# Performance work log

Hardware: AMD Instinct MI355X
Metric: run time of the kernel (lower is better)

The kernel has to match this reference:

```python
import jax, jax.numpy as jnp
import numpy as np

S, D = 4096, 64
DROPOUT_P = 0.1


def setup_inputs() -> dict:
    key = jax.random.key(0)
    k1, k2, k3, k4, k5, k6 = jax.random.split(key, 6)
    return {
        "query": jax.random.normal(k1, (S, D), dtype=jnp.float32),
        "key": jax.random.normal(k2, (S, D), dtype=jnp.float32),
        "value": jax.random.normal(k3, (S, D), dtype=jnp.float32),
        "u_drop": jax.random.uniform(k4, (S, S), dtype=jnp.float32),
        "row_rand": jax.random.uniform(k5, (S, 1), dtype=jnp.float32),
        "x": jax.random.normal(k6, (1,), dtype=jnp.float32),
    }


def reference(query, key, value, u_drop, row_rand, x):
    d = query.shape[-1]
    # torch code divides by scale_factor = d**-0.5, i.e. multiplies by sqrt(d)
    qk = jnp.matmul(query, key.T) * jnp.asarray(d, query.dtype) ** 0.5  # [S,S]
    # dropout with keep prob (1-p), inverted scaling (matches F.dropout)
    keep = (u_drop >= DROPOUT_P).astype(qk.dtype) / (1.0 - DROPOUT_P)
    t = qk * keep  # [S,S]
    # drop_rows_or_cols: random floor mask normalized by its global sum
    r = jnp.floor(t * row_rand)          # [S,S] (row_rand broadcasts over cols)
    t = t * (r / jnp.sum(r))             # [S,S]
    return jnp.matmul(t, value)          # [S,D]
```

## Files before the change

### kernel.cpp

```cpp
#include <hip/hip_runtime.h>
#include <stdint.h>


#define S 4096
#define D 64
#define NCHUNK 8
#define JCHUNK (S / NCHUNK)
#define JT 128
#define NTILES (JCHUNK / JT)
#define LDP 132
#define KSCALE (8.0f / 0.9f)

typedef float f32x4 __attribute__((ext_vector_type(4)));
typedef short s16x8 __attribute__((ext_vector_type(8)));
typedef unsigned short u16x4 __attribute__((ext_vector_type(4)));
typedef const __attribute__((address_space(1))) unsigned g_u32;
typedef __attribute__((address_space(3))) unsigned lds_u32;

__device__ inline unsigned short f2bf(float f) {
    union { float f; unsigned u; } v; v.f = f;
    unsigned r = v.u + 0x7fffu + ((v.u >> 16) & 1u);
    return (unsigned short)(r >> 16);
}

__global__ void prep_all(const float* __restrict__ Q,
                         const float* __restrict__ Kf,
                         const float* __restrict__ V,
                         short* __restrict__ Qbf, short* __restrict__ Kbf,
                         short* __restrict__ VTbf, int* __restrict__ sumr) {
    __shared__ short tile[64 * 68];
    const int b   = blockIdx.x;
    const int tid = threadIdx.x;
    if (b == 0 && tid == 0) *sumr = 0;

    if (b < 512) {
        const int idx = b * 256 + tid;
        if (idx < 65536) {
            float4 v = ((const float4*)Q)[idx];
            u16x4 o; o[0] = f2bf(v.x); o[1] = f2bf(v.y); o[2] = f2bf(v.z); o[3] = f2bf(v.w);
            ((u16x4*)Qbf)[idx] = o;
        } else {
            const int k = idx - 65536;
            float4 v = ((const float4*)Kf)[k];
            u16x4 o; o[0] = f2bf(v.x * KSCALE); o[1] = f2bf(v.y * KSCALE);
                     o[2] = f2bf(v.z * KSCALE); o[3] = f2bf(v.w * KSCALE);
            ((u16x4*)Kbf)[k] = o;
        }
    } else {
        const int j0 = (b - 512) * 64;
#pragma unroll
        for (int it = 0; it < 4; ++it) {
            const int f4 = tid + it * 256;
            const int row = f4 >> 4, c4 = (f4 & 15) * 4;
            float4 v = *(const float4*)&V[(size_t)(j0 + row) * D + c4];
            tile[(c4 + 0) * 68 + row] = (short)f2bf(v.x);
            tile[(c4 + 1) * 68 + row] = (short)f2bf(v.y);
            tile[(c4 + 2) * 68 + row] = (short)f2bf(v.z);
            tile[(c4 + 3) * 68 + row] = (short)f2bf(v.w);
        }
        __syncthreads();
#pragma unroll
        for (int it = 0; it < 4; ++it) {
            const int f4 = tid + it * 256;
            const int d = f4 >> 4, o4 = (f4 & 15) * 4;
            u16x4 w = *(const u16x4*)&tile[d * 68 + o4];
            *(u16x4*)&VTbf[(size_t)d * S + j0 + o4] = w;
        }
    }
}

__launch_bounds__(256, 2)
__global__ void fused_main(const short* __restrict__ Qbf,
                           const short* __restrict__ Kbf,
                           const short* __restrict__ VTbf,
                           const float* __restrict__ Ud,
                           const float* __restrict__ RR,
                           float* __restrict__ Opart,
                           int* __restrict__ sumr)
{
    __shared__ short kb[2][16 * 512];
    __shared__ short vb[16 * 512];
    __shared__ short pb[4 * 16 * LDP];
    __shared__ int red[4];

    const int tid  = threadIdx.x;
    const int w    = tid >> 6;
    const int lane = tid & 63;
    const int quad = lane >> 4;
    const int n16  = lane & 15;

    const int ib  = blockIdx.x & 63;
    const int ic  = blockIdx.x >> 6;
    const int i0w = ib * 64 + w * 16;
    const int jbase = ic * JCHUNK;

    const float* uwb = Ud + (size_t)i0w * S;

    s16x8 aQ[2];
#pragma unroll
    for (int ks = 0; ks < 2; ++ks)
        aQ[ks] = *(const s16x8*)&Qbf[(size_t)(i0w + n16) * D + ks * 32 + quad * 8];

    float rr[4];
#pragma unroll
    for (int rg = 0; rg < 4; ++rg) rr[rg] = RR[i0w + quad * 4 + rg];

    f32x4 accO[4];
#pragma unroll
    for (int ds = 0; ds < 4; ++ds) accO[ds] = (f32x4){0.f, 0.f, 0.f, 0.f};

    float lsum = 0.f;
    short* pw = pb + w * 16 * LDP;

    unsigned um[2];
    const int bsel  = quad * 4 + (n16 & 3);
    const int bidx0 = (n16 >> 2) * 4;

    float4 un[8];
    {
        const int j0 = jbase;
#pragma unroll
        for (int h = 0; h < 2; ++h)
#pragma unroll
            for (int q = 0; q < 4; ++q)
                un[h * 4 + q] = *(const float4*)&uwb[(size_t)(q * 4 + quad) * S + j0 + h * 64 + n16 * 4];
#pragma unroll
        for (int p = 0; p < 4; ++p) {
            const int e = w * 4 + p;
            __builtin_amdgcn_global_load_lds(
                (g_u32*)&Kbf[(size_t)(j0 + (e >> 1) * 16 + n16) * D + (e & 1) * 32 + quad * 8],
                (lds_u32*)&kb[0][e * 512], 16, 0, 0);
        }
#pragma unroll
        for (int p = 0; p < 4; ++p) {
            const int e = w * 4 + p;
            __builtin_amdgcn_global_load_lds(
                (g_u32*)&VTbf[(size_t)((e & 3) * 16 + n16) * S + j0 + (e >> 2) * 32 + quad * 8],
                (lds_u32*)&vb[e * 512], 16, 0, 0);
        }
        unsigned m = 0;
#pragma unroll
        for (int e = 0; e < 8; ++e) {
            m |= (un[e].x >= 0.1f ? 1u : 0u) << (e * 4 + 0);
            m |= (un[e].y >= 0.1f ? 1u : 0u) << (e * 4 + 1);
            m |= (un[e].z >= 0.1f ? 1u : 0u) << (e * 4 + 2);
            m |= (un[e].w >= 0.1f ? 1u : 0u) << (e * 4 + 3);
        }
        um[0] = m;
    }

#pragma unroll
    for (int jt = 0; jt < NTILES; ++jt) {
        const int bu = jt & 1;
        const int nb = bu ^ 1;
        const int j0 = jbase + jt * JT;
        const bool last = (jt + 1 == NTILES);

        if (!last) {
            const int j1 = j0 + JT;
#pragma unroll
            for (int h = 0; h < 2; ++h)
#pragma unroll
                for (int q = 0; q < 4; ++q)
                    un[h * 4 + q] = *(const float4*)&uwb[(size_t)(q * 4 + quad) * S + j1 + h * 64 + n16 * 4];
#pragma unroll
            for (int p = 0; p < 4; ++p) {
                const int e = w * 4 + p;
                __builtin_amdgcn_global_load_lds(
                    (g_u32*)&Kbf[(size_t)(j1 + (e >> 1) * 16 + n16) * D + (e & 1) * 32 + quad * 8],
                    (lds_u32*)&kb[nb][e * 512], 16, 0, 0);
            }
        }

        if (!last) { __asm__ volatile("s_waitcnt vmcnt(12)" ::: "memory"); }
        else       { __asm__ volatile("s_waitcnt vmcnt(0)"  ::: "memory"); }
        __builtin_amdgcn_s_barrier();
        __asm__ volatile("" ::: "memory");

#pragma unroll
        for (int cs = 0; cs < 8; ++cs) {
            f32x4 acc = (f32x4){0.f, 0.f, 0.f, 0.f};
#pragma unroll
            for (int ks = 0; ks < 2; ++ks) {
                s16x8 bK = *(const s16x8*)&kb[bu][(cs * 2 + ks) * 512 + lane * 8];
                acc = __builtin_amdgcn_mfma_f32_16x16x32_bf16(aQ[ks], bK, acc, 0, 0, 0);
            }
            const int h = cs >> 2, c4 = cs & 3;
#pragma unroll
            for (int rg = 0; rg < 4; ++rg) {
                const int mv = __builtin_amdgcn_ds_bpermute(
                    (rg * 16 + c4 * 4) * 4 + bidx0, (int)um[bu]);
                const float t = ((((unsigned)mv) >> (h * 16 + bsel)) & 1u) ? acc[rg] : 0.0f;
                const float r = floorf(t * rr[rg]);
                lsum += r;
                pw[(quad * 4 + rg) * LDP + cs * 16 + n16] = (short)f2bf(t * r);
            }
        }

        __builtin_amdgcn_wave_barrier();
        __asm__ volatile("s_waitcnt lgkmcnt(0)" ::: "memory");
        __builtin_amdgcn_wave_barrier();

#pragma unroll
        for (int ksj = 0; ksj < 4; ++ksj) {
            s16x8 aP = *(const s16x8*)&pw[n16 * LDP + ksj * 32 + quad * 8];
#pragma unroll
            for (int ds = 0; ds < 4; ++ds) {
                s16x8 bV = *(const s16x8*)&vb[(ksj * 4 + ds) * 512 + lane * 8];
                accO[ds] = __builtin_amdgcn_mfma_f32_16x16x32_bf16(aP, bV, accO[ds], 0, 0, 0);
            }
        }

        __asm__ volatile("" ::: "memory");
        __builtin_amdgcn_s_barrier();
        __asm__ volatile("" ::: "memory");

        if (!last) {
            unsigned m = 0;
#pragma unroll
            for (int e = 0; e < 8; ++e) {
                m |= (un[e].x >= 0.1f ? 1u : 0u) << (e * 4 + 0);
                m |= (un[e].y >= 0.1f ? 1u : 0u) << (e * 4 + 1);
                m |= (un[e].z >= 0.1f ? 1u : 0u) << (e * 4 + 2);
                m |= (un[e].w >= 0.1f ? 1u : 0u) << (e * 4 + 3);
            }
            um[nb] = m;
            const int j1 = j0 + JT;
#pragma unroll
            for (int p = 0; p < 4; ++p) {
                const int e = w * 4 + p;
                __builtin_amdgcn_global_load_lds(
                    (g_u32*)&VTbf[(size_t)((e & 3) * 16 + n16) * S + j1 + (e >> 2) * 32 + quad * 8],
                    (lds_u32*)&vb[e * 512], 16, 0, 0);
            }
        }
    }

    float* op = Opart + (size_t)ic * S * D;
#pragma unroll
    for (int ds = 0; ds < 4; ++ds) {
        const int d = ds * 16 + n16;
#pragma unroll
        for (int rg = 0; rg < 4; ++rg) {
            const int i = i0w + quad * 4 + rg;
            op[(size_t)i * D + d] = accO[ds][rg];
        }
    }

    for (int off = 32; off; off >>= 1) lsum += __shfl_down(lsum, off);
    if (lane == 0) red[w] = (int)lsum;
    __syncthreads();
    if (tid == 0) atomicAdd(sumr, red[0] + red[1] + red[2] + red[3]);
}

__global__ void reduce_out(const float* __restrict__ Opart,
                           const int* __restrict__ sumr,
                           float* __restrict__ out) {
    const int idx = blockIdx.x * 256 + threadIdx.x;
    const float invR = 1.0f / (float)(*sumr);
    float sx = 0.f, sy = 0.f, sz = 0.f, sw = 0.f;
#pragma unroll
    for (int c = 0; c < NCHUNK; ++c) {
        const float4 v = ((const float4*)(Opart + (size_t)c * S * D))[idx];
        sx += v.x; sy += v.y; sz += v.z; sw += v.w;
    }
    float4 o; o.x = sx * invR; o.y = sy * invR; o.z = sz * invR; o.w = sw * invR;
    ((float4*)out)[idx] = o;
}

extern "C" void kernel_launch(void* const* d_in, const int* in_sizes, int n_in,
                              void* d_out, int out_size, void* d_ws, size_t ws_size,
                              hipStream_t stream) {
    (void)in_sizes; (void)n_in; (void)out_size; (void)ws_size;
    const float* Q  = (const float*)d_in[0];
    const float* Kf = (const float*)d_in[1];
    const float* V  = (const float*)d_in[2];
    const float* Ud = (const float*)d_in[3];
    const float* RR = (const float*)d_in[4];
    float* out = (float*)d_out;

    char* ws = (char*)d_ws;
    float* Opart = (float*)ws;
    short* Qbf  = (short*)(ws + (8u << 20));
    short* Kbf  = (short*)(ws + (8u << 20) + (512u << 10));
    short* VTbf = (short*)(ws + (8u << 20) + (1024u << 10));
    int*   sumr = (int*)  (ws + (8u << 20) + (1536u << 10));

    prep_all<<<dim3(576), dim3(256), 0, stream>>>(Q, Kf, V, Qbf, Kbf, VTbf, sumr);
    fused_main<<<dim3(64 * NCHUNK), dim3(256), 0, stream>>>(
        Qbf, Kbf, VTbf, Ud, RR, Opart, sumr);
    reduce_out<<<dim3(256), dim3(256), 0, stream>>>(Opart, sumr, out);
}
```

Before: 121.2 us.

## Pre-pack dropout mask into bitmask in prep kernel, read bits in main kernel

```diff
diff --git a/kernel.cpp b/kernel.cpp
--- a/kernel.cpp
+++ b/kernel.cpp
@@ -10,10 +10,12 @@
 #define NTILES (JCHUNK / JT)
 #define LDP 132
 #define KSCALE (8.0f / 0.9f)
+#define MASKB 2048
 
 typedef float f32x4 __attribute__((ext_vector_type(4)));
 typedef short s16x8 __attribute__((ext_vector_type(8)));
 typedef unsigned short u16x4 __attribute__((ext_vector_type(4)));
+typedef int i32x4 __attribute__((ext_vector_type(4)));
 typedef const __attribute__((address_space(1))) unsigned g_u32;
 typedef __attribute__((address_space(3))) unsigned lds_u32;
 
@@ -26,15 +28,30 @@
 __global__ void prep_all(const float* __restrict__ Q,
                          const float* __restrict__ Kf,
                          const float* __restrict__ V,
+                         const float* __restrict__ Ud,
                          short* __restrict__ Qbf, short* __restrict__ Kbf,
-                         short* __restrict__ VTbf, int* __restrict__ sumr) {
+                         short* __restrict__ VTbf,
+                         unsigned* __restrict__ PM, int* __restrict__ sumr) {
     __shared__ short tile[64 * 68];
     const int b   = blockIdx.x;
     const int tid = threadIdx.x;
     if (b == 0 && tid == 0) *sumr = 0;
 
-    if (b < 512) {
-        const int idx = b * 256 + tid;
+    if (b < MASKB) {
+        const int wi = b * 256 + tid;
+        const float4* src = (const float4*)Ud + (size_t)wi * 8;
+        unsigned m = 0;
+#pragma unroll
+        for (int q = 0; q < 8; ++q) {
+            const float4 v = src[q];
+            m |= (v.x >= 0.1f ? 1u : 0u) << (q * 4 + 0);
+            m |= (v.y >= 0.1f ? 1u : 0u) << (q * 4 + 1);
+            m |= (v.z >= 0.1f ? 1u : 0u) << (q * 4 + 2);
+            m |= (v.w >= 0.1f ? 1u : 0u) << (q * 4 + 3);
+        }
+        PM[wi] = m;
+    } else if (b < MASKB + 512) {
+        const int idx = (b - MASKB) * 256 + tid;
         if (idx < 65536) {
             float4 v = ((const float4*)Q)[idx];
             u16x4 o; o[0] = f2bf(v.x); o[1] = f2bf(v.y); o[2] = f2bf(v.z); o[3] = f2bf(v.w);
@@ -47,7 +64,7 @@
             ((u16x4*)Kbf)[k] = o;
         }
     } else {
-        const int j0 = (b - 512) * 64;
+        const int j0 = (b - MASKB - 512) * 64;
 #pragma unroll
         for (int it = 0; it < 4; ++it) {
             const int f4 = tid + it * 256;
@@ -73,7 +90,7 @@
 __global__ void fused_main(const short* __restrict__ Qbf,
                            const short* __restrict__ Kbf,
                            const short* __restrict__ VTbf,
-                           const float* __restrict__ Ud,
+                           const unsigned* __restrict__ PM,
                            const float* __restrict__ RR,
                            float* __restrict__ Opart,
                            int* __restrict__ sumr)
@@ -94,8 +111,6 @@
     const int i0w = ib * 64 + w * 16;
     const int jbase = ic * JCHUNK;
 
-    const float* uwb = Ud + (size_t)i0w * S;
-
     s16x8 aQ[2];
 #pragma unroll
     for (int ks = 0; ks < 2; ++ks)
@@ -112,41 +127,31 @@
     float lsum = 0.f;
     short* pw = pb + w * 16 * LDP;
 
-    unsigned um[2];
-    const int bsel  = quad * 4 + (n16 & 3);
-    const int bidx0 = (n16 >> 2) * 4;
-
-    float4 un[8];
+    const unsigned* pmr[4];
+#pragma unroll
+    for (int rg = 0; rg < 4; ++rg)
+        pmr[rg] = PM + (size_t)(i0w + quad * 4 + rg) * (S / 32) + (jbase >> 5);
+
+    i32x4 mk[2][4];
+
     {
-        const int j0 = jbase;
-#pragma unroll
-        for (int h = 0; h < 2; ++h)
-#pragma unroll
-            for (int q = 0; q < 4; ++q)
-                un[h * 4 + q] = *(const float4*)&uwb[(size_t)(q * 4 + quad) * S + j0 + h * 64 + n16 * 4];
+#pragma unroll
+        for (int rg = 0; rg < 4; ++rg)
+            mk[0][rg] = *(const i32x4*)pmr[rg];
 #pragma unroll
         for (int p = 0; p < 4; ++p) {
             const int e = w * 4 + p;
             __builtin_amdgcn_global_load_lds(
-                (g_u32*)&Kbf[(size_t)(j0 + (e >> 1) * 16 + n16) * D + (e & 1) * 32 + quad * 8],
+                (g_u32*)&Kbf[(size_t)(jbase + (e >> 1) * 16 + n16) * D + (e & 1) * 32 + quad * 8],
                 (lds_u32*)&kb[0][e * 512], 16, 0, 0);
         }
 #pragma unroll
         for (int p = 0; p < 4; ++p) {
             const int e = w * 4 + p;
             __builtin_amdgcn_global_load_lds(
-                (g_u32*)&VTbf[(size_t)((e & 3) * 16 + n16) * S + j0 + (e >> 2) * 32 + quad * 8],
+                (g_u32*)&VTbf[(size_t)((e & 3) * 16 + n16) * S + jbase + (e >> 2) * 32 + quad * 8],
                 (lds_u32*)&vb[e * 512], 16, 0, 0);
         }
-        unsigned m = 0;
-#pragma unroll
-        for (int e = 0; e < 8; ++e) {
-            m |= (un[e].x >= 0.1f ? 1u : 0u) << (e * 4 + 0);
-            m |= (un[e].y >= 0.1f ? 1u : 0u) << (e * 4 + 1);
-            m |= (un[e].z >= 0.1f ? 1u : 0u) << (e * 4 + 2);
-            m |= (un[e].w >= 0.1f ? 1u : 0u) << (e * 4 + 3);
-        }
-        um[0] = m;
     }
 
 #pragma unroll
@@ -159,10 +164,8 @@
         if (!last) {
             const int j1 = j0 + JT;
 #pragma unroll
-            for (int h = 0; h < 2; ++h)
-#pragma unroll
-                for (int q = 0; q < 4; ++q)
-                    un[h * 4 + q] = *(const float4*)&uwb[(size_t)(q * 4 + quad) * S + j1 + h * 64 + n16 * 4];
+            for (int rg = 0; rg < 4; ++rg)
+                mk[nb][rg] = *(const i32x4*)(pmr[rg] + ((jt + 1) * (JT / 32)));
 #pragma unroll
             for (int p = 0; p < 4; ++p) {
                 const int e = w * 4 + p;
@@ -172,8 +175,8 @@
             }
         }
 
-        if (!last) { __asm__ volatile("s_waitcnt vmcnt(12)" ::: "memory"); }
-        else       { __asm__ volatile("s_waitcnt vmcnt(0)"  ::: "memory"); }
+        if (!last) { __asm__ volatile("s_waitcnt vmcnt(8)" ::: "memory"); }
+        else       { __asm__ volatile("s_waitcnt vmcnt(0)" ::: "memory"); }
         __builtin_amdgcn_s_barrier();
         __asm__ volatile("" ::: "memory");
 
@@ -185,12 +188,12 @@
                 s16x8 bK = *(const s16x8*)&kb[bu][(cs * 2 + ks) * 512 + lane * 8];
                 acc = __builtin_amdgcn_mfma_f32_16x16x32_bf16(aQ[ks], bK, acc, 0, 0, 0);
             }
-            const int h = cs >> 2, c4 = cs & 3;
+            const int wsel = cs >> 1;
+            const int sh = (cs & 1) * 16 + n16;
 #pragma unroll
             for (int rg = 0; rg < 4; ++rg) {
-                const int mv = __builtin_amdgcn_ds_bpermute(
-                    (rg * 16 + c4 * 4) * 4 + bidx0, (int)um[bu]);
-                const float t = ((((unsigned)mv) >> (h * 16 + bsel)) & 1u) ? acc[rg] : 0.0f;
+                const unsigned word = (unsigned)mk[bu][rg][wsel];
+                const float t = ((word >> sh) & 1u) ? acc[rg] : 0.0f;
                 const float r = floorf(t * rr[rg]);
                 lsum += r;
                 pw[(quad * 4 + rg) * LDP + cs * 16 + n16] = (short)f2bf(t * r);
@@ -216,15 +219,6 @@
         __asm__ volatile("" ::: "memory");
 
         if (!last) {
-            unsigned m = 0;
-#pragma unroll
-            for (int e = 0; e < 8; ++e) {
-                m |= (un[e].x >= 0.1f ? 1u : 0u) << (e * 4 + 0);
-                m |= (un[e].y >= 0.1f ? 1u : 0u) << (e * 4 + 1);
-                m |= (un[e].z >= 0.1f ? 1u : 0u) << (e * 4 + 2);
-                m |= (un[e].w >= 0.1f ? 1u : 0u) << (e * 4 + 3);
-            }
-            um[nb] = m;
             const int j1 = j0 + JT;
 #pragma unroll
             for (int p = 0; p < 4; ++p) {
@@ -285,9 +279,10 @@
     short* Kbf  = (short*)(ws + (8u << 20) + (512u << 10));
     short* VTbf = (short*)(ws + (8u << 20) + (1024u << 10));
     int*   sumr = (int*)  (ws + (8u << 20) + (1536u << 10));
-
-    prep_all<<<dim3(576), dim3(256), 0, stream>>>(Q, Kf, V, Qbf, Kbf, VTbf, sumr);
+    unsigned* PM = (unsigned*)(ws + (8u << 20) + (1664u << 10));
+
+    prep_all<<<dim3(MASKB + 576), dim3(256), 0, stream>>>(Q, Kf, V, Ud, Qbf, Kbf, VTbf, PM, sumr);
     fused_main<<<dim3(64 * NCHUNK), dim3(256), 0, stream>>>(
-        Qbf, Kbf, VTbf, Ud, RR, Opart, sumr);
+        Qbf, Kbf, VTbf, PM, RR, Opart, sumr);
     reduce_out<<<dim3(256), dim3(256), 0, stream>>>(Opart, sumr, out);
 }
```

New measurement: 129.3 us. +6.7%, slower.

## Keep P in registers via transposed QK MFMA and bpermute, double-buffer V

Applied to the files above, without the earlier changes.

```diff
diff --git a/kernel.cpp b/kernel.cpp
--- a/kernel.cpp
+++ b/kernel.cpp
@@ -8,12 +8,12 @@
 #define JCHUNK (S / NCHUNK)
 #define JT 128
 #define NTILES (JCHUNK / JT)
-#define LDP 132
 #define KSCALE (8.0f / 0.9f)
 
 typedef float f32x4 __attribute__((ext_vector_type(4)));
 typedef short s16x8 __attribute__((ext_vector_type(8)));
 typedef unsigned short u16x4 __attribute__((ext_vector_type(4)));
+typedef int i32x4 __attribute__((ext_vector_type(4)));
 typedef const __attribute__((address_space(1))) unsigned g_u32;
 typedef __attribute__((address_space(3))) unsigned lds_u32;
 
@@ -21,6 +21,12 @@
     union { float f; unsigned u; } v; v.f = f;
     unsigned r = v.u + 0x7fffu + ((v.u >> 16) & 1u);
     return (unsigned short)(r >> 16);
+}
+
+__device__ inline unsigned cvt_pk_bf16(float lo, float hi) {
+    unsigned r;
+    asm("v_cvt_pk_bf16_f32 %0, %1, %2" : "=v"(r) : "v"(lo), "v"(hi));
+    return r;
 }
 
 __global__ void prep_all(const float* __restrict__ Q,
@@ -79,8 +85,7 @@
                            int* __restrict__ sumr)
 {
     __shared__ short kb[2][16 * 512];
-    __shared__ short vb[16 * 512];
-    __shared__ short pb[4 * 16 * LDP];
+    __shared__ short vb[2][16 * 512];
     __shared__ int red[4];
 
     const int tid  = threadIdx.x;
@@ -94,75 +99,54 @@
     const int i0w = ib * 64 + w * 16;
     const int jbase = ic * JCHUNK;
 
-    const float* uwb = Ud + (size_t)i0w * S;
+    const float* uln = Ud + (size_t)(i0w + n16) * S + quad * 4;
 
     s16x8 aQ[2];
 #pragma unroll
     for (int ks = 0; ks < 2; ++ks)
         aQ[ks] = *(const s16x8*)&Qbf[(size_t)(i0w + n16) * D + ks * 32 + quad * 8];
 
-    float rr[4];
-#pragma unroll
-    for (int rg = 0; rg < 4; ++rg) rr[rg] = RR[i0w + quad * 4 + rg];
+    const float rrn = RR[i0w + n16];
 
     f32x4 accO[4];
 #pragma unroll
     for (int ds = 0; ds < 4; ++ds) accO[ds] = (f32x4){0.f, 0.f, 0.f, 0.f};
 
     float lsum = 0.f;
-    short* pw = pb + w * 16 * LDP;
-
-    unsigned um[2];
-    const int bsel  = quad * 4 + (n16 & 3);
-    const int bidx0 = (n16 >> 2) * 4;
-
     float4 un[8];
+    unsigned um;
+
     {
-        const int j0 = jbase;
-#pragma unroll
-        for (int h = 0; h < 2; ++h)
-#pragma unroll
-            for (int q = 0; q < 4; ++q)
-                un[h * 4 + q] = *(const float4*)&uwb[(size_t)(q * 4 + quad) * S + j0 + h * 64 + n16 * 4];
 #pragma unroll
         for (int p = 0; p < 4; ++p) {
             const int e = w * 4 + p;
             __builtin_amdgcn_global_load_lds(
-                (g_u32*)&Kbf[(size_t)(j0 + (e >> 1) * 16 + n16) * D + (e & 1) * 32 + quad * 8],
+                (g_u32*)&Kbf[(size_t)(jbase + (e >> 1) * 16 + n16) * D + (e & 1) * 32 + quad * 8],
                 (lds_u32*)&kb[0][e * 512], 16, 0, 0);
         }
 #pragma unroll
         for (int p = 0; p < 4; ++p) {
             const int e = w * 4 + p;
             __builtin_amdgcn_global_load_lds(
-                (g_u32*)&VTbf[(size_t)((e & 3) * 16 + n16) * S + j0 + (e >> 2) * 32 + quad * 8],
-                (lds_u32*)&vb[e * 512], 16, 0, 0);
-        }
-        unsigned m = 0;
-#pragma unroll
-        for (int e = 0; e < 8; ++e) {
-            m |= (un[e].x >= 0.1f ? 1u : 0u) << (e * 4 + 0);
-            m |= (un[e].y >= 0.1f ? 1u : 0u) << (e * 4 + 1);
-            m |= (un[e].z >= 0.1f ? 1u : 0u) << (e * 4 + 2);
-            m |= (un[e].w >= 0.1f ? 1u : 0u) << (e * 4 + 3);
-        }
-        um[0] = m;
+                (g_u32*)&VTbf[(size_t)((e & 3) * 16 + n16) * S + jbase + (e >> 2) * 32 + quad * 8],
+                (lds_u32*)&vb[0][e * 512], 16, 0, 0);
+        }
+#pragma unroll
+        for (int c = 0; c < 8; ++c)
+            un[c] = *(const float4*)&uln[jbase + c * 16];
+        __asm__ volatile("s_waitcnt vmcnt(8)" ::: "memory");
+        __builtin_amdgcn_s_barrier();
+        __asm__ volatile("" ::: "memory");
     }
 
 #pragma unroll
     for (int jt = 0; jt < NTILES; ++jt) {
         const int bu = jt & 1;
         const int nb = bu ^ 1;
-        const int j0 = jbase + jt * JT;
         const bool last = (jt + 1 == NTILES);
 
         if (!last) {
-            const int j1 = j0 + JT;
-#pragma unroll
-            for (int h = 0; h < 2; ++h)
-#pragma unroll
-                for (int q = 0; q < 4; ++q)
-                    un[h * 4 + q] = *(const float4*)&uwb[(size_t)(q * 4 + quad) * S + j1 + h * 64 + n16 * 4];
+            const int j1 = jbase + (jt + 1) * JT;
 #pragma unroll
             for (int p = 0; p < 4; ++p) {
                 const int e = w * 4 + p;
@@ -170,69 +154,78 @@
                     (g_u32*)&Kbf[(size_t)(j1 + (e >> 1) * 16 + n16) * D + (e & 1) * 32 + quad * 8],
                     (lds_u32*)&kb[nb][e * 512], 16, 0, 0);
             }
-        }
-
-        if (!last) { __asm__ volatile("s_waitcnt vmcnt(12)" ::: "memory"); }
-        else       { __asm__ volatile("s_waitcnt vmcnt(0)"  ::: "memory"); }
-        __builtin_amdgcn_s_barrier();
-        __asm__ volatile("" ::: "memory");
-
-#pragma unroll
-        for (int cs = 0; cs < 8; ++cs) {
-            f32x4 acc = (f32x4){0.f, 0.f, 0.f, 0.f};
-#pragma unroll
-            for (int ks = 0; ks < 2; ++ks) {
-                s16x8 bK = *(const s16x8*)&kb[bu][(cs * 2 + ks) * 512 + lane * 8];
-                acc = __builtin_amdgcn_mfma_f32_16x16x32_bf16(aQ[ks], bK, acc, 0, 0, 0);
-            }
-            const int h = cs >> 2, c4 = cs & 3;
-#pragma unroll
-            for (int rg = 0; rg < 4; ++rg) {
-                const int mv = __builtin_amdgcn_ds_bpermute(
-                    (rg * 16 + c4 * 4) * 4 + bidx0, (int)um[bu]);
-                const float t = ((((unsigned)mv) >> (h * 16 + bsel)) & 1u) ? acc[rg] : 0.0f;
-                const float r = floorf(t * rr[rg]);
-                lsum += r;
-                pw[(quad * 4 + rg) * LDP + cs * 16 + n16] = (short)f2bf(t * r);
-            }
-        }
-
-        __builtin_amdgcn_wave_barrier();
-        __asm__ volatile("s_waitcnt lgkmcnt(0)" ::: "memory");
-        __builtin_amdgcn_wave_barrier();
-
-#pragma unroll
-        for (int ksj = 0; ksj < 4; ++ksj) {
-            s16x8 aP = *(const s16x8*)&pw[n16 * LDP + ksj * 32 + quad * 8];
-#pragma unroll
-            for (int ds = 0; ds < 4; ++ds) {
-                s16x8 bV = *(const s16x8*)&vb[(ksj * 4 + ds) * 512 + lane * 8];
-                accO[ds] = __builtin_amdgcn_mfma_f32_16x16x32_bf16(aP, bV, accO[ds], 0, 0, 0);
-            }
-        }
-
-        __asm__ volatile("" ::: "memory");
-        __builtin_amdgcn_s_barrier();
-        __asm__ volatile("" ::: "memory");
-
-        if (!last) {
-            unsigned m = 0;
-#pragma unroll
-            for (int e = 0; e < 8; ++e) {
-                m |= (un[e].x >= 0.1f ? 1u : 0u) << (e * 4 + 0);
-                m |= (un[e].y >= 0.1f ? 1u : 0u) << (e * 4 + 1);
-                m |= (un[e].z >= 0.1f ? 1u : 0u) << (e * 4 + 2);
-                m |= (un[e].w >= 0.1f ? 1u : 0u) << (e * 4 + 3);
-            }
-            um[nb] = m;
-            const int j1 = j0 + JT;
 #pragma unroll
             for (int p = 0; p < 4; ++p) {
                 const int e = w * 4 + p;
                 __builtin_amdgcn_global_load_lds(
                     (g_u32*)&VTbf[(size_t)((e & 3) * 16 + n16) * S + j1 + (e >> 2) * 32 + quad * 8],
-                    (lds_u32*)&vb[e * 512], 16, 0, 0);
-            }
+                    (lds_u32*)&vb[nb][e * 512], 16, 0, 0);
+            }
+        }
+
+        {
+            unsigned m = 0;
+#pragma unroll
+            for (int c = 0; c < 8; ++c) {
+                m |= (un[c].x >= 0.1f ? 1u : 0u) << (c * 4 + 0);
+                m |= (un[c].y >= 0.1f ? 1u : 0u) << (c * 4 + 1);
+                m |= (un[c].z >= 0.1f ? 1u : 0u) << (c * 4 + 2);
+                m |= (un[c].w >= 0.1f ? 1u : 0u) << (c * 4 + 3);
+            }
+            um = m;
+        }
+        if (!last) {
+            const int j1 = jbase + (jt + 1) * JT;
+#pragma unroll
+            for (int c = 0; c < 8; ++c)
+                un[c] = *(const float4*)&uln[j1 + c * 16];
+        }
+
+        unsigned pkw[16];
+#pragma unroll
+        for (int cs = 0; cs < 8; ++cs) {
+            f32x4 acc = (f32x4){0.f, 0.f, 0.f, 0.f};
+#pragma unroll
+            for (int ks = 0; ks < 2; ++ks) {
+                s16x8 bK = *(const s16x8*)&kb[bu][(cs * 2 + ks) * 512 + lane * 8];
+                acc = __builtin_amdgcn_mfma_f32_16x16x32_bf16(bK, aQ[ks], acc, 0, 0, 0);
+            }
+            float vv[4];
+#pragma unroll
+            for (int rg = 0; rg < 4; ++rg) {
+                const float t = ((um >> (cs * 4 + rg)) & 1u) ? acc[rg] : 0.0f;
+                const float r = floorf(t * rrn);
+                lsum += r;
+                vv[rg] = t * r;
+            }
+            pkw[cs * 2]     = cvt_pk_bf16(vv[0], vv[1]);
+            pkw[cs * 2 + 1] = cvt_pk_bf16(vv[2], vv[3]);
+        }
+
+        const int pbase = (32 * ((lane >> 4) & 1) + n16) * 4;
+#pragma unroll
+        for (int ksj = 0; ksj < 4; ++ksj) {
+            i32x4 aw;
+#pragma unroll
+            for (int widx = 0; widx < 4; ++widx) {
+                const int addr = pbase + (widx >> 1) * 64;
+                const int lo = __builtin_amdgcn_ds_bpermute(addr, (int)pkw[ksj * 4 + (widx & 1)]);
+                const int hi = __builtin_amdgcn_ds_bpermute(addr, (int)pkw[ksj * 4 + 2 + (widx & 1)]);
+                aw[widx] = (lane >= 32) ? hi : lo;
+            }
+            s16x8 aP;
+            __builtin_memcpy(&aP, &aw, 16);
+#pragma unroll
+            for (int ds = 0; ds < 4; ++ds) {
+                s16x8 bV = *(const s16x8*)&vb[bu][(ksj * 4 + ds) * 512 + lane * 8];
+                accO[ds] = __builtin_amdgcn_mfma_f32_16x16x32_bf16(aP, bV, accO[ds], 0, 0, 0);
+            }
+        }
+
+        if (!last) {
+            __asm__ volatile("s_waitcnt vmcnt(8)" ::: "memory");
+            __builtin_amdgcn_s_barrier();
+            __asm__ volatile("" ::: "memory");
         }
     }
 
```

Measured after the change: 120.9 us. Within noise of the previous version (-0.3%).
